# Kernel optimization log

Hardware: AMD Instinct MI355X
Metric: run time of the kernel (lower is better)

## Reference

```python
import jax, jax.numpy as jnp
import numpy as np

B, L, D_MODEL, H = 4, 2048, 1024, 16
HD = D_MODEL // H  # head_dim = 64


def _rope_tables(seq_len, dim, dtype):
    inv_freq = 1.0 / (10000.0 ** (jnp.arange(0, dim, 2, dtype=jnp.float32) / dim))
    t = jnp.arange(seq_len, dtype=jnp.float32)
    freqs = jnp.outer(t, inv_freq)  # (S, dim/2)
    return jnp.cos(freqs).astype(dtype), jnp.sin(freqs).astype(dtype)


def _apply_rope(x):
    # x: (B, H, S, d)
    cos, sin = _rope_tables(x.shape[-2], x.shape[-1], x.dtype)  # (S, d/2)
    x_even = x[..., 0::2]
    x_odd = x[..., 1::2]
    out_even = x_even * cos - x_odd * sin
    out_odd = x_even * sin + x_odd * cos
    return jnp.stack([out_even, out_odd], axis=-1).reshape(x.shape)


def setup_inputs() -> dict:
    key = jax.random.key(0)
    ks = jax.random.split(key, 9)
    s = 1.0 / np.sqrt(D_MODEL)
    inp = {
        "query": jax.random.normal(ks[0], (B, L, D_MODEL), dtype=jnp.float32),
        "Wq": jax.random.uniform(ks[1], (D_MODEL, D_MODEL), jnp.float32, -s, s),
        "bq": jax.random.uniform(ks[2], (D_MODEL,), jnp.float32, -s, s),
        "Wk": jax.random.uniform(ks[3], (D_MODEL, D_MODEL), jnp.float32, -s, s),
        "bk": jax.random.uniform(ks[4], (D_MODEL,), jnp.float32, -s, s),
        "Wv": jax.random.uniform(ks[5], (D_MODEL, D_MODEL), jnp.float32, -s, s),
        "bv": jax.random.uniform(ks[6], (D_MODEL,), jnp.float32, -s, s),
        "Wo": jax.random.uniform(ks[7], (D_MODEL, D_MODEL), jnp.float32, -s, s),
        "bo": jax.random.uniform(ks[8], (D_MODEL,), jnp.float32, -s, s),
    }
    return inp


def reference(query, Wq, bq, Wk, bk, Wv, bv, Wo, bo):
    Bq, Lq, _ = query.shape
    # projections (torch Linear: x @ W.T + b), split into heads -> (B, H, L, d)
    def proj(x, W, b):
        y = x @ W.T + b
        return y.reshape(Bq, Lq, H, HD).transpose(0, 2, 1, 3)
    q = _apply_rope(proj(query, Wq, bq))
    k = _apply_rope(proj(query, Wk, bk))
    v = proj(query, Wv, bv)
    scores = jnp.einsum("bhqd,bhkd->bhqk", q, k) / np.sqrt(HD)
    causal_mask = jnp.triu(jnp.ones((Lq, Lq), dtype=bool), k=1)
    scores = jnp.where(causal_mask[None, None, :, :], -jnp.inf, scores)
    attn = jax.nn.softmax(scores, axis=-1)
    out = jnp.einsum("bhqk,bhkd->bhqd", attn, v)
    out = out.transpose(0, 2, 1, 3).reshape(Bq, Lq, D_MODEL)
    return out @ Wo.T + bo
```

## Files before the change

kernel.cpp:

```cpp
#include <hip/hip_runtime.h>
#include <hip/hip_bf16.h>
#include <math.h>

#define L_SEQ  2048
#define DMODEL 1024
#define NHEAD  16
#define HEADD  64

typedef __attribute__((ext_vector_type(8))) short short8;
typedef __attribute__((ext_vector_type(4))) short short4v;
typedef __attribute__((ext_vector_type(4))) float f32x4;

#define LDA 32

static __device__ __forceinline__ unsigned short f2bf(float f) {
    unsigned int u = __float_as_uint(f);
    unsigned int r = (u + 0x7fffu + ((u >> 16) & 1u)) >> 16;
    return (unsigned short)r;
}

static __device__ __forceinline__ void dma16(const unsigned short* g, unsigned short* l) {
    __builtin_amdgcn_global_load_lds((const __attribute__((address_space(1))) void*)g,
                                     (__attribute__((address_space(3))) void*)l, 16, 0, 0);
}

__global__ void cvt_f32_bf16(const float* __restrict__ in,
                             unsigned short* __restrict__ out, int n4) {
    int i = blockIdx.x * blockDim.x + threadIdx.x;
    if (i >= n4) return;
    float4 v = reinterpret_cast<const float4*>(in)[i];
    ushort4 o;
    o.x = f2bf(v.x); o.y = f2bf(v.y); o.z = f2bf(v.z); o.w = f2bf(v.w);
    reinterpret_cast<ushort4*>(out)[i] = o;
}

__global__ void cvt_weights(const float* __restrict__ Wq, const float* __restrict__ Wk,
                            const float* __restrict__ Wv, const float* __restrict__ Wo,
                            unsigned short* __restrict__ dst) {
    int i = blockIdx.x * blockDim.x + threadIdx.x;
    int which = i >> 18;
    const float* src = which == 0 ? Wq : which == 1 ? Wk : which == 2 ? Wv : Wo;
    float4 v = reinterpret_cast<const float4*>(src)[i & 262143];
    ushort4 o;
    o.x = f2bf(v.x); o.y = f2bf(v.y); o.z = f2bf(v.z); o.w = f2bf(v.w);
    reinterpret_cast<ushort4*>(dst)[i] = o;
}

__global__ void build_rope(float* __restrict__ tab) {
    int i = blockIdx.x * blockDim.x + threadIdx.x;
    int lpos = i >> 5, i2 = i & 31;
    float inv_f = expf(-0.28782313662425574f * (float)i2);
    float ang = (float)lpos * inv_f;
    tab[2 * i]     = cosf(ang);
    tab[2 * i + 1] = sinf(ang);
}

#define BKP 32

__global__ __launch_bounds__(256) void proj_qkv(
    const unsigned short* __restrict__ X,
    const unsigned short* __restrict__ Wqkv,
    const float* __restrict__ bq_,
    const float* __restrict__ bk_,
    const float* __restrict__ bv_,
    const float* __restrict__ rope,
    unsigned short* __restrict__ Qb,
    unsigned short* __restrict__ Kb,
    unsigned short* __restrict__ Vr)
{
    __shared__ unsigned short a_lds[3][128 * BKP];
    __shared__ unsigned short b_lds[3][128 * BKP];

    const int tid  = threadIdx.x;
    const int lane = tid & 63;
    const int w    = tid >> 6;
    const int wm   = w & 1, wn = w >> 1;
    const int quad = lane >> 4, l16 = lane & 15;

    const int orig = blockIdx.y * 24 + blockIdx.x;
    const int swz  = (orig & 7) * 192 + (orig >> 3);
    const int bx   = swz % 24;
    const int by   = swz / 24;
    const int m0   = by * 128;
    const int n0   = bx * 128;

    const int sel = bx >> 3;
    const float* bias   = sel == 0 ? bq_ : (sel == 1 ? bk_ : bv_);
    unsigned short* out = sel == 0 ? Qb  : (sel == 1 ? Kb  : Vr);

    const int st_row = lane >> 2;
    const int st_col = (((lane & 3) ^ ((lane >> 3) & 3)) << 3);
    const int rd = ((quad ^ ((l16 >> 1) & 3)) << 3);

    f32x4 acc[4][4];
#pragma unroll
    for (int i = 0; i < 4; ++i)
#pragma unroll
        for (int j = 0; j < 4; ++j) acc[i][j] = (f32x4){0.f, 0.f, 0.f, 0.f};

    const unsigned short* Xs = X    + (size_t)(m0 + w * 32 + st_row) * DMODEL + st_col;
    const unsigned short* Ws = Wqkv + (size_t)(n0 + w * 32 + st_row) * DMODEL + st_col;
    const int ldsA0 = (w * 32) * BKP, ldsA1 = (w * 32 + 16) * BKP;

#pragma unroll
    for (int p = 0; p < 2; ++p) {
        const int kk = p * BKP;
        dma16(Xs + kk,               &a_lds[p][ldsA0]);
        dma16(Xs + 16 * DMODEL + kk, &a_lds[p][ldsA1]);
        dma16(Ws + kk,               &b_lds[p][ldsA0]);
        dma16(Ws + 16 * DMODEL + kk, &b_lds[p][ldsA1]);
    }
    asm volatile("s_waitcnt vmcnt(4)" ::: "memory");
    __builtin_amdgcn_s_barrier();

    for (int kt = 0; kt < 32; ++kt) {
        const int slot = kt % 3;
        const int ps   = (kt + 2) % 3;
        const int kk   = ((kt + 2) & 31) * BKP;

        short8 af[4], bf[2];
#pragma unroll
        for (int i = 0; i < 4; ++i)
            af[i] = *reinterpret_cast<const short8*>(
                &a_lds[slot][(wm * 64 + i * 16 + l16) * BKP + rd]);
#pragma unroll
        for (int j = 0; j < 2; ++j)
            bf[j] = *reinterpret_cast<const short8*>(
                &b_lds[slot][(wn * 64 + j * 16 + l16) * BKP + rd]);
        dma16(Xs + kk,               &a_lds[ps][ldsA0]);
        dma16(Xs + 16 * DMODEL + kk, &a_lds[ps][ldsA1]);
        __builtin_amdgcn_s_barrier();
        asm volatile("s_waitcnt lgkmcnt(0)" ::: "memory");
        __builtin_amdgcn_sched_barrier(0);
        __builtin_amdgcn_s_setprio(1);
#pragma unroll
        for (int i = 0; i < 4; ++i)
#pragma unroll
            for (int j = 0; j < 2; ++j)
                acc[i][j] = __builtin_amdgcn_mfma_f32_16x16x32_bf16(af[i], bf[j], acc[i][j], 0, 0, 0);
        __builtin_amdgcn_s_setprio(0);
        __builtin_amdgcn_s_barrier();

#pragma unroll
        for (int j = 0; j < 2; ++j)
            bf[j] = *reinterpret_cast<const short8*>(
                &b_lds[slot][(wn * 64 + (2 + j) * 16 + l16) * BKP + rd]);
        dma16(Ws + kk,               &b_lds[ps][ldsA0]);
        dma16(Ws + 16 * DMODEL + kk, &b_lds[ps][ldsA1]);
        __builtin_amdgcn_s_barrier();
        asm volatile("s_waitcnt lgkmcnt(0)" ::: "memory");
        __builtin_amdgcn_sched_barrier(0);
        __builtin_amdgcn_s_setprio(1);
#pragma unroll
        for (int i = 0; i < 4; ++i)
#pragma unroll
            for (int j = 0; j < 2; ++j)
                acc[i][2 + j] = __builtin_amdgcn_mfma_f32_16x16x32_bf16(af[i], bf[j], acc[i][2 + j], 0, 0, 0);
        __builtin_amdgcn_s_setprio(0);
        asm volatile("s_waitcnt vmcnt(4)" ::: "memory");
        __builtin_amdgcn_s_barrier();
    }
    asm volatile("s_waitcnt vmcnt(0)" ::: "memory");

#pragma unroll
    for (int jf = 0; jf < 4; ++jf) {
        int nn = (bx & 7) * 128 + wn * 64 + jf * 16 + l16;
        float bval = bias[nn];
        int d  = nn & (HEADD - 1);
        int h  = nn >> 6;
        float sgn = (d & 1) ? 1.0f : -1.0f;
        int i2 = d >> 1;
#pragma unroll
        for (int mf = 0; mf < 4; ++mf) {
#pragma unroll
            for (int r = 0; r < 4; ++r) {
                int m_g = m0 + wm * 64 + mf * 16 + quad * 4 + r;
                float v = acc[mf][jf][r] + bval;
                int b    = m_g >> 11;
                int lpos = m_g & (L_SEQ - 1);
                if (sel < 2) {
                    float p = __shfl_xor(v, 1);
                    float2 cs = *reinterpret_cast<const float2*>(&rope[(size_t)(lpos * 32 + i2) * 2]);
                    v = v * cs.x + sgn * cs.y * p;
                    if (sel == 0) v *= 0.18033688011112042f;
                }
                out[((size_t)(b * NHEAD + h) * L_SEQ + lpos) * HEADD + d] = f2bf(v);
            }
        }
    }
}

__global__ __launch_bounds__(256) void transpose_v(
    const unsigned short* __restrict__ Vr, unsigned short* __restrict__ Vt)
{
    __shared__ unsigned short tile[64 * 72];
    const int tid = threadIdx.x;
    const int bh  = blockIdx.y;
    const int l0  = blockIdx.x * 64;
#pragma unroll
    for (int t = 0; t < 2; ++t) {
        int c = tid + t * 256;
        int row = c >> 3, cc = (c & 7) << 3;
        int4 v = *reinterpret_cast<const int4*>(Vr + ((size_t)bh * L_SEQ + l0 + row) * HEADD + cc);
        *reinterpret_cast<int4*>(&tile[row * 72 + cc]) = v;
    }
    __syncthreads();
#pragma unroll
    for (int t = 0; t < 2; ++t) {
        int c = tid + t * 256;
        int d = c >> 3, lc = (c & 7) << 3;
        union { unsigned short u[8]; int4 v; } tt;
#pragma unroll
        for (int j = 0; j < 8; ++j) tt.u[j] = tile[(lc + j) * 72 + d];
        *reinterpret_cast<int4*>(Vt + ((size_t)bh * HEADD + d) * L_SEQ + l0 + lc) = tt.v;
    }
}

__global__ __launch_bounds__(256) void attn_fwd(
    const unsigned short* __restrict__ Q,
    const unsigned short* __restrict__ K,
    const unsigned short* __restrict__ Vt,
    unsigned short* __restrict__ Oa)
{
    __shared__ unsigned short k_lds[2][64 * 64];
    __shared__ unsigned short v_lds[2][64 * 64];
    const int tid  = threadIdx.x;
    const int lane = tid & 63;
    const int w    = tid >> 6;
    const int quad = lane >> 4, l16 = lane & 15;
    const int pair = blockIdx.y;
    const int bh   = blockIdx.x;
    const size_t base = (size_t)bh * L_SEQ * HEADD;
    const int b = bh >> 4, h = bh & 15;

    const int srow  = lane >> 3;
    const int sslot = lane & 7;
    const int ssw   = ((sslot ^ srow) << 3);
    const unsigned short* Ksrc = K  + base + (size_t)(w * 8 + srow) * HEADD  + ssw;
    const unsigned short* Vsrc = Vt + base + (size_t)(w * 8 + srow) * L_SEQ + ssw;
    const int d0 = (w * 8) * 64;
    const int d1 = (32 + w * 8) * 64;
    const int swr = (l16 & 7);

    for (int half = 0; half < 2; ++half) {
        const int qb = half ? (31 - pair) : pair;
        const int qrow = qb * 64 + w * 16 + l16;

        short8 qf[2];
#pragma unroll
        for (int ks = 0; ks < 2; ++ks)
            qf[ks] = *reinterpret_cast<const short8*>(Q + base + (size_t)qrow * HEADD + ks * 32 + quad * 8);

        f32x4 o[4];
#pragma unroll
        for (int nt = 0; nt < 4; ++nt) o[nt] = (f32x4){0.f, 0.f, 0.f, 0.f};
        float lsum = 0.f;

        dma16(Ksrc,                 &k_lds[0][d0]);
        dma16(Ksrc + 32 * HEADD,    &k_lds[0][d1]);
        dma16(Vsrc,                 &v_lds[0][d0]);
        dma16(Vsrc + 32 * L_SEQ,    &v_lds[0][d1]);
        asm volatile("s_waitcnt vmcnt(0)" ::: "memory");
        __builtin_amdgcn_s_barrier();

        int cur = 0;
        for (int kb = 0; kb <= qb; ++kb) {
            const int kn = (kb + 1) <= qb ? (kb + 1) : 0;
            const int nb = cur ^ 1;
            dma16(Ksrc + (size_t)(kn * 64) * HEADD,        &k_lds[nb][d0]);
            dma16(Ksrc + (size_t)(kn * 64 + 32) * HEADD,   &k_lds[nb][d1]);
            dma16(Vsrc + kn * 64,                          &v_lds[nb][d0]);
            dma16(Vsrc + kn * 64 + 32 * L_SEQ,             &v_lds[nb][d1]);

            f32x4 st[4];
#pragma unroll
            for (int nt = 0; nt < 4; ++nt) st[nt] = (f32x4){0.f, 0.f, 0.f, 0.f};
            __builtin_amdgcn_s_setprio(1);
#pragma unroll
            for (int ks = 0; ks < 2; ++ks)
#pragma unroll
                for (int nt = 0; nt < 4; ++nt) {
                    short8 kf = *reinterpret_cast<const short8*>(
                        &k_lds[cur][(nt * 16 + l16) * 64 + (((ks * 4 + quad) ^ swr) << 3)]);
                    st[nt] = __builtin_amdgcn_mfma_f32_16x16x32_bf16(kf, qf[ks], st[nt], 0, 0, 0);
                }
            __builtin_amdgcn_s_setprio(0);

            if (kb == qb) {
#pragma unroll
                for (int nt = 0; nt < 4; ++nt)
#pragma unroll
                    for (int r = 0; r < 4; ++r) {
                        int seqcol = kb * 64 + nt * 16 + quad * 4 + r;
                        if (seqcol > qrow) st[nt][r] = -INFINITY;
                    }
            }

            short4v pfrag[4];
#pragma unroll
            for (int nt = 0; nt < 4; ++nt) {
                float p0 = __builtin_amdgcn_exp2f(st[nt][0]);
                float p1 = __builtin_amdgcn_exp2f(st[nt][1]);
                float p2 = __builtin_amdgcn_exp2f(st[nt][2]);
                float p3 = __builtin_amdgcn_exp2f(st[nt][3]);
                lsum += (p0 + p1) + (p2 + p3);
                unsigned u0 = __float_as_uint(p0) + 0x8000u;
                unsigned u1 = __float_as_uint(p1) + 0x8000u;
                unsigned u2 = __float_as_uint(p2) + 0x8000u;
                unsigned u3 = __float_as_uint(p3) + 0x8000u;
                union { unsigned u[2]; short4v v; } pk;
                pk.u[0] = (u0 >> 16) | (u1 & 0xffff0000u);
                pk.u[1] = (u2 >> 16) | (u3 & 0xffff0000u);
                pfrag[nt] = pk.v;
            }

            __builtin_amdgcn_s_setprio(1);
#pragma unroll
            for (int c = 0; c < 4; ++c)
#pragma unroll
                for (int nt2 = 0; nt2 < 4; ++nt2) {
                    short4v vf = *reinterpret_cast<const short4v*>(
                        &v_lds[cur][(nt2 * 16 + l16) * 64 +
                                    (((c * 2 + (quad >> 1)) ^ swr) << 3) + ((quad & 1) << 2)]);
                    o[nt2] = __builtin_amdgcn_mfma_f32_16x16x16bf16_1k(pfrag[c], vf, o[nt2], 0, 0, 0);
                }
            __builtin_amdgcn_s_setprio(0);

            asm volatile("s_waitcnt vmcnt(0)" ::: "memory");
            __builtin_amdgcn_s_barrier();
            cur ^= 1;
        }

        lsum += __shfl_xor(lsum, 16);
        lsum += __shfl_xor(lsum, 32);
        float rs[4];
#pragma unroll
        for (int r = 0; r < 4; ++r) rs[r] = __shfl(lsum, quad * 4 + r);
#pragma unroll
        for (int r = 0; r < 4; ++r) {
            float inv = 1.0f / rs[r];
            int lg = qb * 64 + w * 16 + quad * 4 + r;
#pragma unroll
            for (int nt = 0; nt < 4; ++nt) {
                int d = nt * 16 + l16;
                Oa[(size_t)(b * L_SEQ + lg) * DMODEL + h * HEADD + d] = f2bf(o[nt][r] * inv);
            }
        }
    }
}

__global__ __launch_bounds__(256) void out_gemm(
    const unsigned short* __restrict__ X,
    const unsigned short* __restrict__ W,
    const float* __restrict__ bias,
    float* __restrict__ out)
{
    __shared__ unsigned short a_lds[3][128 * BKP];
    __shared__ unsigned short b_lds[3][128 * BKP];
    const int tid  = threadIdx.x;
    const int lane = tid & 63;
    const int w    = tid >> 6;
    const int wm   = w & 1, wn = w >> 1;
    const int quad = lane >> 4, l16 = lane & 15;

    const int orig = blockIdx.y * 8 + blockIdx.x;
    const int swz  = (orig & 7) * 64 + (orig >> 3);
    const int m0 = (swz >> 3) * 128;
    const int n0 = (swz & 7) * 128;

    const int st_row = lane >> 2;
    const int st_col = (((lane & 3) ^ ((lane >> 3) & 3)) << 3);
    const int rd = ((quad ^ ((l16 >> 1) & 3)) << 3);

    f32x4 acc[4][4];
#pragma unroll
    for (int i = 0; i < 4; ++i)
#pragma unroll
        for (int j = 0; j < 4; ++j) acc[i][j] = (f32x4){0.f, 0.f, 0.f, 0.f};

    const unsigned short* Xs = X + (size_t)(m0 + w * 32 + st_row) * DMODEL + st_col;
    const unsigned short* Ws = W + (size_t)(n0 + w * 32 + st_row) * DMODEL + st_col;
    const int ldsA0 = (w * 32) * BKP, ldsA1 = (w * 32 + 16) * BKP;

#pragma unroll
    for (int p = 0; p < 2; ++p) {
        const int kk = p * BKP;
        dma16(Xs + kk,               &a_lds[p][ldsA0]);
        dma16(Xs + 16 * DMODEL + kk, &a_lds[p][ldsA1]);
        dma16(Ws + kk,               &b_lds[p][ldsA0]);
        dma16(Ws + 16 * DMODEL + kk, &b_lds[p][ldsA1]);
    }
    asm volatile("s_waitcnt vmcnt(4)" ::: "memory");
    __builtin_amdgcn_s_barrier();

    for (int kt = 0; kt < 32; ++kt) {
        const int slot = kt % 3;
        const int ps   = (kt + 2) % 3;
        const int kk   = ((kt + 2) & 31) * BKP;

        dma16(Xs + kk,               &a_lds[ps][ldsA0]);
        dma16(Xs + 16 * DMODEL + kk, &a_lds[ps][ldsA1]);
        dma16(Ws + kk,               &b_lds[ps][ldsA0]);
        dma16(Ws + 16 * DMODEL + kk, &b_lds[ps][ldsA1]);

        short8 af[4], bf[4];
#pragma unroll
        for (int i = 0; i < 4; ++i)
            af[i] = *reinterpret_cast<const short8*>(
                &a_lds[slot][(wm * 64 + i * 16 + l16) * BKP + rd]);
#pragma unroll
        for (int j = 0; j < 4; ++j)
            bf[j] = *reinterpret_cast<const short8*>(
                &b_lds[slot][(wn * 64 + j * 16 + l16) * BKP + rd]);
        asm volatile("s_waitcnt lgkmcnt(0)" ::: "memory");
        __builtin_amdgcn_sched_barrier(0);
        __builtin_amdgcn_s_setprio(1);
#pragma unroll
        for (int i = 0; i < 4; ++i)
#pragma unroll
            for (int j = 0; j < 4; ++j)
                acc[i][j] = __builtin_amdgcn_mfma_f32_16x16x32_bf16(af[i], bf[j], acc[i][j], 0, 0, 0);
        __builtin_amdgcn_s_setprio(0);
        asm volatile("s_waitcnt vmcnt(4)" ::: "memory");
        __builtin_amdgcn_s_barrier();
    }
    asm volatile("s_waitcnt vmcnt(0)" ::: "memory");

#pragma unroll
    for (int nt = 0; nt < 4; ++nt) {
        int n_g = n0 + wn * 64 + nt * 16 + l16;
        float bv = bias[n_g];
#pragma unroll
        for (int mt = 0; mt < 4; ++mt)
#pragma unroll
            for (int r = 0; r < 4; ++r) {
                int m_g = m0 + wm * 64 + mt * 16 + quad * 4 + r;
                out[(size_t)m_g * DMODEL + n_g] = acc[mt][nt][r] + bv;
            }
    }
}

extern "C" void kernel_launch(void* const* d_in, const int* in_sizes, int n_in,
                              void* d_out, int out_size, void* d_ws, size_t ws_size,
                              hipStream_t stream) {
    const float* query = (const float*)d_in[0];
    const float* Wq = (const float*)d_in[1];
    const float* bq = (const float*)d_in[2];
    const float* Wk = (const float*)d_in[3];
    const float* bk = (const float*)d_in[4];
    const float* Wv = (const float*)d_in[5];
    const float* bv = (const float*)d_in[6];
    const float* Wo = (const float*)d_in[7];
    const float* bo = (const float*)d_in[8];
    float* out = (float*)d_out;

    unsigned short* ws  = (unsigned short*)d_ws;
    unsigned short* xb  = ws;
    unsigned short* wqb = xb  + (size_t)8388608;
    unsigned short* wkb = wqb + 1048576;
    unsigned short* wvb = wkb + 1048576;
    unsigned short* wob = wvb + 1048576;
    unsigned short* Qb  = wob + 1048576;
    unsigned short* Kb  = Qb  + 8388608;
    unsigned short* Vr  = Kb  + 8388608;
    unsigned short* Vtb = Vr  + 8388608;
    unsigned short* Ab  = Vtb + 8388608;
    float* rope = (float*)(Ab + 8388608);

    (void)wkb; (void)wvb;

    build_rope<<<256, 256, 0, stream>>>(rope);
    cvt_f32_bf16<<<8192, 256, 0, stream>>>(query, xb, 2097152);
    cvt_weights<<<4096, 256, 0, stream>>>(Wq, Wk, Wv, Wo, wqb);

    proj_qkv<<<dim3(24, 64), 256, 0, stream>>>(xb, wqb, bq, bk, bv, rope, Qb, Kb, Vr);
    transpose_v<<<dim3(32, 64), 256, 0, stream>>>(Vr, Vtb);
    attn_fwd<<<dim3(64, 16), 256, 0, stream>>>(Qb, Kb, Vtb, Ab);
    out_gemm<<<dim3(8, 64), 256, 0, stream>>>(Ab, wob, bo, out);
}
```

Measured before the change: 295.7 us.

## Fuse V transpose into QKV projection epilogue via LDS-staged vectorized stores

The QKV projection epilogue now stages results in the reused LDS pool and writes them out with 16-byte vector stores. V tiles are written transposed directly into the head-major (d, L) layout. This removes the separate transpose_v kernel and its extra global read and write of V. It also replaces scattered 2-byte stores with coalesced wide stores, at the cost of an extra LDS round trip and barriers in the epilogue.

```diff
diff --git a/kernel.cpp b/kernel.cpp
--- a/kernel.cpp
+++ b/kernel.cpp
@@ -10,8 +10,6 @@
 typedef __attribute__((ext_vector_type(8))) short short8;
 typedef __attribute__((ext_vector_type(4))) short short4v;
 typedef __attribute__((ext_vector_type(4))) float f32x4;
-
-#define LDA 32
 
 static __device__ __forceinline__ unsigned short f2bf(float f) {
     unsigned int u = __float_as_uint(f);
@@ -68,8 +66,9 @@
     unsigned short* __restrict__ Kb,
     unsigned short* __restrict__ Vr)
 {
-    __shared__ unsigned short a_lds[3][128 * BKP];
-    __shared__ unsigned short b_lds[3][128 * BKP];
+    __shared__ unsigned short pool[24576];
+    unsigned short* a_ring = pool;
+    unsigned short* b_ring = pool + 12288;
 
     const int tid  = threadIdx.x;
     const int lane = tid & 63;
@@ -105,30 +104,30 @@
 #pragma unroll
     for (int p = 0; p < 2; ++p) {
         const int kk = p * BKP;
-        dma16(Xs + kk,               &a_lds[p][ldsA0]);
-        dma16(Xs + 16 * DMODEL + kk, &a_lds[p][ldsA1]);
-        dma16(Ws + kk,               &b_lds[p][ldsA0]);
-        dma16(Ws + 16 * DMODEL + kk, &b_lds[p][ldsA1]);
+        dma16(Xs + kk,               a_ring + p * 4096 + ldsA0);
+        dma16(Xs + 16 * DMODEL + kk, a_ring + p * 4096 + ldsA1);
+        dma16(Ws + kk,               b_ring + p * 4096 + ldsA0);
+        dma16(Ws + 16 * DMODEL + kk, b_ring + p * 4096 + ldsA1);
     }
     asm volatile("s_waitcnt vmcnt(4)" ::: "memory");
     __builtin_amdgcn_s_barrier();
 
     for (int kt = 0; kt < 32; ++kt) {
-        const int slot = kt % 3;
-        const int ps   = (kt + 2) % 3;
+        const int slot = (kt % 3) * 4096;
+        const int ps   = ((kt + 2) % 3) * 4096;
         const int kk   = ((kt + 2) & 31) * BKP;
 
         short8 af[4], bf[2];
 #pragma unroll
         for (int i = 0; i < 4; ++i)
             af[i] = *reinterpret_cast<const short8*>(
-                &a_lds[slot][(wm * 64 + i * 16 + l16) * BKP + rd]);
+                &a_ring[slot + (wm * 64 + i * 16 + l16) * BKP + rd]);
 #pragma unroll
         for (int j = 0; j < 2; ++j)
             bf[j] = *reinterpret_cast<const short8*>(
-                &b_lds[slot][(wn * 64 + j * 16 + l16) * BKP + rd]);
-        dma16(Xs + kk,               &a_lds[ps][ldsA0]);
-        dma16(Xs + 16 * DMODEL + kk, &a_lds[ps][ldsA1]);
+                &b_ring[slot + (wn * 64 + j * 16 + l16) * BKP + rd]);
+        dma16(Xs + kk,               a_ring + ps + ldsA0);
+        dma16(Xs + 16 * DMODEL + kk, a_ring + ps + ldsA1);
         __builtin_amdgcn_s_barrier();
         asm volatile("s_waitcnt lgkmcnt(0)" ::: "memory");
         __builtin_amdgcn_sched_barrier(0);
@@ -144,9 +143,9 @@
 #pragma unroll
         for (int j = 0; j < 2; ++j)
             bf[j] = *reinterpret_cast<const short8*>(
-                &b_lds[slot][(wn * 64 + (2 + j) * 16 + l16) * BKP + rd]);
-        dma16(Ws + kk,               &b_lds[ps][ldsA0]);
-        dma16(Ws + 16 * DMODEL + kk, &b_lds[ps][ldsA1]);
+                &b_ring[slot + (wn * 64 + (2 + j) * 16 + l16) * BKP + rd]);
+        dma16(Ws + kk,               b_ring + ps + ldsA0);
+        dma16(Ws + 16 * DMODEL + kk, b_ring + ps + ldsA1);
         __builtin_amdgcn_s_barrier();
         asm volatile("s_waitcnt lgkmcnt(0)" ::: "memory");
         __builtin_amdgcn_sched_barrier(0);
@@ -161,58 +160,54 @@
         __builtin_amdgcn_s_barrier();
     }
     asm volatile("s_waitcnt vmcnt(0)" ::: "memory");
+    __builtin_amdgcn_s_barrier();
 
 #pragma unroll
     for (int jf = 0; jf < 4; ++jf) {
-        int nn = (bx & 7) * 128 + wn * 64 + jf * 16 + l16;
+        int nl = wn * 64 + jf * 16 + l16;
+        int nn = (bx & 7) * 128 + nl;
         float bval = bias[nn];
         int d  = nn & (HEADD - 1);
-        int h  = nn >> 6;
         float sgn = (d & 1) ? 1.0f : -1.0f;
         int i2 = d >> 1;
 #pragma unroll
         for (int mf = 0; mf < 4; ++mf) {
 #pragma unroll
             for (int r = 0; r < 4; ++r) {
-                int m_g = m0 + wm * 64 + mf * 16 + quad * 4 + r;
+                int ml = wm * 64 + mf * 16 + quad * 4 + r;
+                int lpos = (m0 + ml) & (L_SEQ - 1);
                 float v = acc[mf][jf][r] + bval;
-                int b    = m_g >> 11;
-                int lpos = m_g & (L_SEQ - 1);
                 if (sel < 2) {
                     float p = __shfl_xor(v, 1);
                     float2 cs = *reinterpret_cast<const float2*>(&rope[(size_t)(lpos * 32 + i2) * 2]);
                     v = v * cs.x + sgn * cs.y * p;
                     if (sel == 0) v *= 0.18033688011112042f;
                 }
-                out[((size_t)(b * NHEAD + h) * L_SEQ + lpos) * HEADD + d] = f2bf(v);
+                pool[(sel < 2) ? (ml * 136 + nl) : (nl * 136 + ml)] = f2bf(v);
             }
         }
     }
-}
-
-__global__ __launch_bounds__(256) void transpose_v(
-    const unsigned short* __restrict__ Vr, unsigned short* __restrict__ Vt)
-{
-    __shared__ unsigned short tile[64 * 72];
-    const int tid = threadIdx.x;
-    const int bh  = blockIdx.y;
-    const int l0  = blockIdx.x * 64;
-#pragma unroll
-    for (int t = 0; t < 2; ++t) {
-        int c = tid + t * 256;
-        int row = c >> 3, cc = (c & 7) << 3;
-        int4 v = *reinterpret_cast<const int4*>(Vr + ((size_t)bh * L_SEQ + l0 + row) * HEADD + cc);
-        *reinterpret_cast<int4*>(&tile[row * 72 + cc]) = v;
-    }
-    __syncthreads();
-#pragma unroll
-    for (int t = 0; t < 2; ++t) {
-        int c = tid + t * 256;
-        int d = c >> 3, lc = (c & 7) << 3;
-        union { unsigned short u[8]; int4 v; } tt;
-#pragma unroll
-        for (int j = 0; j < 8; ++j) tt.u[j] = tile[(lc + j) * 72 + d];
-        *reinterpret_cast<int4*>(Vt + ((size_t)bh * HEADD + d) * L_SEQ + l0 + lc) = tt.v;
+    __builtin_amdgcn_s_barrier();
+
+    const int b     = m0 >> 11;
+    const int lpos0 = m0 & (L_SEQ - 1);
+#pragma unroll
+    for (int i = 0; i < 8; ++i) {
+        int g   = i * 256 + tid;
+        int row = g >> 4;
+        int c8  = (g & 15) * 8;
+        int4 val = *reinterpret_cast<const int4*>(&pool[row * 136 + c8]);
+        size_t addr;
+        if (sel < 2) {
+            int n_g = (bx & 7) * 128 + c8;
+            int h = n_g >> 6, d = n_g & 63;
+            addr = ((size_t)(b * NHEAD + h) * L_SEQ + (lpos0 + row)) * HEADD + d;
+        } else {
+            int n_g = (bx & 7) * 128 + row;
+            int h = n_g >> 6, d = n_g & 63;
+            addr = ((size_t)(b * NHEAD + h) * HEADD + d) * L_SEQ + lpos0 + c8;
+        }
+        *reinterpret_cast<int4*>(out + addr) = val;
     }
 }
 
@@ -349,6 +344,8 @@
     }
 }
 
+#define LDA 32
+
 __global__ __launch_bounds__(256) void out_gemm(
     const unsigned short* __restrict__ X,
     const unsigned short* __restrict__ W,
@@ -463,8 +460,7 @@
     unsigned short* Qb  = wob + 1048576;
     unsigned short* Kb  = Qb  + 8388608;
     unsigned short* Vr  = Kb  + 8388608;
-    unsigned short* Vtb = Vr  + 8388608;
-    unsigned short* Ab  = Vtb + 8388608;
+    unsigned short* Ab  = Vr  + 8388608;
     float* rope = (float*)(Ab + 8388608);
 
     (void)wkb; (void)wvb;
@@ -474,7 +470,6 @@
     cvt_weights<<<4096, 256, 0, stream>>>(Wq, Wk, Wv, Wo, wqb);
 
     proj_qkv<<<dim3(24, 64), 256, 0, stream>>>(xb, wqb, bq, bk, bv, rope, Qb, Kb, Vr);
-    transpose_v<<<dim3(32, 64), 256, 0, stream>>>(Vr, Vtb);
-    attn_fwd<<<dim3(64, 16), 256, 0, stream>>>(Qb, Kb, Vtb, Ab);
+    attn_fwd<<<dim3(64, 16), 256, 0, stream>>>(Qb, Kb, Vr, Ab);
     out_gemm<<<dim3(8, 64), 256, 0, stream>>>(Ab, wob, bo, out);
 }
```

Result: faster. 288.3 us (-2.5%).
